# Kernel optimization log

Hardware: AMD Instinct MI355X
Metric: run time of the kernel (lower is better)

## Reference

```python
import jax, jax.numpy as jnp
import numpy as np

HEADS = 16
DIM_HEAD = 64
SCALE = DIM_HEAD ** -0.5
LN_EPS = 1e-5


def setup_inputs() -> dict:
    key = jax.random.key(0)
    k1, k2, k3 = jax.random.split(key, 3)
    b, s, d = 2, 2048, 1024
    inner = HEADS * DIM_HEAD
    x = jax.random.normal(k1, (b, s, d), dtype=jnp.float32)
    w_qkv = jax.random.normal(k2, (d, 3 * inner), dtype=jnp.float32) * (d ** -0.5)
    w_out = jax.random.normal(k3, (inner, d), dtype=jnp.float32) * (inner ** -0.5)
    return {
        "x": x,
        "ln_gamma": jnp.ones((d,), jnp.float32),
        "ln_beta": jnp.zeros((d,), jnp.float32),
        "w_qkv": w_qkv,
        "w_out": w_out,
        "b_out": jnp.zeros((d,), jnp.float32),
    }


def _layernorm(x, gamma, beta):
    mu = jnp.mean(x, axis=-1, keepdims=True)
    var = jnp.var(x, axis=-1, keepdims=True)
    return (x - mu) * jax.lax.rsqrt(var + LN_EPS) * gamma + beta


def reference(x, ln_gamma, ln_beta, w_qkv, w_out, b_out):
    b, s, d = x.shape
    xn = _layernorm(x, ln_gamma, ln_beta)
    qkv = xn @ w_qkv                       # [b, s, 3*inner]
    q, k, v = jnp.split(qkv, 3, axis=-1)
    def heads(t):
        return t.reshape(b, s, HEADS, DIM_HEAD).transpose(0, 2, 1, 3)  # [b, h, s, dh]
    q, k, v = heads(q), heads(k), heads(v)
    dots = jnp.einsum("bhqd,bhkd->bhqk", q, k) * SCALE   # [b, h, s, s]
    attn = jax.nn.softmax(dots, axis=-1)
    out = jnp.einsum("bhqk,bhkd->bhqd", attn, v)          # [b, h, s, dh]
    out = out.transpose(0, 2, 1, 3).reshape(b, s, HEADS * DIM_HEAD)
    return out @ w_out + b_out
```

## Files before the change

kernel.cpp:

```cpp
#include <hip/hip_runtime.h>
#include <hip/hip_bf16.h>
#include <stdint.h>

#define NH     16
#define DHEAD  64
#define SEQ    2048
#define DMODEL 1024
#define NBATCH 2
#define INNER  1024
#define QKVN   3072
#define ROWS   4096
#define ATT_QB 64
#define ATT_KB 64

typedef __attribute__((ext_vector_type(8))) __bf16 bf16x8;
typedef __attribute__((ext_vector_type(4))) float floatx4;
typedef __attribute__((ext_vector_type(16))) float floatx16;

__device__ __forceinline__ unsigned short f2bf(float f) {
    union { __bf16 b; unsigned short u; } c; c.b = (__bf16)f; return c.u;
}

__device__ __forceinline__ unsigned int pk2(float lo, float hi) {
    union { ushort2 s; unsigned int u; } c;
    c.s.x = f2bf(lo); c.s.y = f2bf(hi); return c.u;
}

__device__ __forceinline__ float fexp2(float x) {
#if __has_builtin(__builtin_amdgcn_exp2f)
    return __builtin_amdgcn_exp2f(x);
#else
    float r; asm("v_exp_f32 %0, %1" : "=v"(r) : "v"(x)); return r;
#endif
}

typedef __attribute__((address_space(1))) void gvoid;
typedef __attribute__((address_space(3))) void lvoid;
__device__ __forceinline__ void gl_lds16(const void* g, void* l) {
    __builtin_amdgcn_global_load_lds((gvoid*)g, (lvoid*)l, 16, 0, 0);
}

__global__ __launch_bounds__(256) void transpose_f2b(
        const float* __restrict__ in, unsigned short* __restrict__ out,
        int rows, int cols) {
    __shared__ unsigned short tile[32][33];
    const int bx = blockIdx.x * 32, by = blockIdx.y * 32;
    const int tx = threadIdx.x & 31, ty = threadIdx.x >> 5;
    for (int i = ty; i < 32; i += 8)
        tile[i][tx] = f2bf(in[(size_t)(by + i) * cols + bx + tx]);
    __syncthreads();
    for (int i = ty; i < 32; i += 8)
        out[(size_t)(bx + i) * rows + by + tx] = tile[tx][i];
}

__global__ __launch_bounds__(256) void ln_kernel(
        const float* __restrict__ x,
        const float* __restrict__ gamma,
        const float* __restrict__ beta,
        unsigned short* __restrict__ xn) {
    __shared__ float red[4][2];
    const int row = blockIdx.x, t = threadIdx.x;
    const size_t base = (size_t)row * DMODEL + t * 4;
    float4 v = *(const float4*)(x + base);
    float s  = v.x + v.y + v.z + v.w;
    float ss = v.x*v.x + v.y*v.y + v.z*v.z + v.w*v.w;
    for (int off = 32; off >= 1; off >>= 1) {
        s  += __shfl_xor(s,  off);
        ss += __shfl_xor(ss, off);
    }
    const int w = t >> 6, lane = t & 63;
    if (lane == 0) { red[w][0] = s; red[w][1] = ss; }
    __syncthreads();
    if (t == 0) {
        float S  = red[0][0] + red[1][0] + red[2][0] + red[3][0];
        float SS = red[0][1] + red[1][1] + red[2][1] + red[3][1];
        float mu  = S * (1.f / DMODEL);
        float var = SS * (1.f / DMODEL) - mu * mu;
        red[0][0] = mu; red[0][1] = rsqrtf(var + 1e-5f);
    }
    __syncthreads();
    const float mu = red[0][0], rstd = red[0][1];
    float4 g = *(const float4*)(gamma + t * 4);
    float4 bb = *(const float4*)(beta + t * 4);
    ushort4 o;
    o.x = f2bf((v.x - mu) * rstd * g.x + bb.x);
    o.y = f2bf((v.y - mu) * rstd * g.y + bb.y);
    o.z = f2bf((v.z - mu) * rstd * g.z + bb.z);
    o.w = f2bf((v.w - mu) * rstd * g.w + bb.w);
    *(ushort4*)(xn + base) = o;
}

__global__ __launch_bounds__(256) void gemm_qkv(
        const unsigned short* __restrict__ A,
        const unsigned short* __restrict__ Bt,
        unsigned short* __restrict__ qP,
        unsigned short* __restrict__ kP,
        unsigned short* __restrict__ vT) {
    const int K = DMODEL;
    __shared__ __align__(16) unsigned short sA[128 * 32];
    __shared__ __align__(16) unsigned short sB[128 * 32];
    __shared__ __align__(16) unsigned short tb[2][64 * 72];
    const int t = threadIdx.x;
    const int mBase = blockIdx.y * 128, nBase = blockIdx.x * 128;
    const int w = t >> 6, lane = t & 63, quad = lane >> 4, l16 = lane & 15;
    const int wm = (w >> 1) * 64, wn = (w & 1) * 64;
    const int srow = t >> 2, sch = t & 3;
    floatx4 acc[4][4];
    for (int mi = 0; mi < 4; mi++)
        for (int ni = 0; ni < 4; ni++) acc[mi][ni] = (floatx4)0.f;

    for (int k0 = 0; k0 < K; k0 += 32) {
        #pragma unroll
        for (int c = 0; c < 2; c++) {
            const int row = c * 64 + srow;
            const int gcol = (sch ^ ((row >> 1) & 3)) * 8;
            gl_lds16(&A[(size_t)(mBase + row) * K + k0 + gcol], &sA[(c * 256 + w * 64) * 8]);
            gl_lds16(&Bt[(size_t)(nBase + row) * K + k0 + gcol], &sB[(c * 256 + w * 64) * 8]);
        }
        __syncthreads();
        bf16x8 af[4], bfv[4];
        #pragma unroll
        for (int mi = 0; mi < 4; mi++) {
            const int r = wm + mi * 16 + l16;
            af[mi] = *(const bf16x8*)&sA[r * 32 + (quad ^ ((r >> 1) & 3)) * 8];
        }
        #pragma unroll
        for (int ni = 0; ni < 4; ni++) {
            const int r = wn + ni * 16 + l16;
            bfv[ni] = *(const bf16x8*)&sB[r * 32 + (quad ^ ((r >> 1) & 3)) * 8];
        }
        #pragma unroll
        for (int mi = 0; mi < 4; mi++)
            #pragma unroll
            for (int ni = 0; ni < 4; ni++)
                acc[mi][ni] = __builtin_amdgcn_mfma_f32_16x16x32_bf16(
                    af[mi], bfv[ni], acc[mi][ni], 0, 0, 0);
        __syncthreads();
    }
    const int reg = nBase >> 10;
    if (reg == 2) {
        #pragma unroll
        for (int ni = 0; ni < 4; ni++) {
            const int col = nBase + wn + ni * 16 + l16;
            const int h = (col & 1023) >> 6, dh = col & 63;
            #pragma unroll
            for (int mi = 0; mi < 4; mi++) {
                const int row0 = mBase + wm + mi * 16 + quad * 4;
                const int b = row0 >> 11, s0 = row0 & 2047;
                ushort4 o;
                o.x = f2bf(acc[mi][ni][0]); o.y = f2bf(acc[mi][ni][1]);
                o.z = f2bf(acc[mi][ni][2]); o.w = f2bf(acc[mi][ni][3]);
                *(ushort4*)&vT[((size_t)(b * NH + h) * DHEAD + dh) * SEQ + s0] = o;
            }
        }
    } else {
        unsigned short* dst = (reg == 0) ? qP : kP;
        const float scl = (reg == 0) ? 0.18033688011112042f : 1.f;
        const int hh = ((nBase + wn) & 1023) >> 6;
        #pragma unroll
        for (int ph = 0; ph < 2; ph++) {
            if ((w >> 1) == ph) {
                unsigned short* tb_ = &tb[w & 1][0];
                #pragma unroll
                for (int mi = 0; mi < 4; mi++)
                    #pragma unroll
                    for (int ni = 0; ni < 4; ni++)
                        #pragma unroll
                        for (int i = 0; i < 4; i++)
                            tb_[(mi * 16 + quad * 4 + i) * 72 + ni * 16 + l16] =
                                f2bf(acc[mi][ni][i] * scl);
                asm volatile("s_waitcnt lgkmcnt(0)" ::: "memory");
                const int row_g = mBase + wm + lane;
                const int b = row_g >> 11, sr = row_g & 2047;
                unsigned short* orow = dst + ((size_t)(b * NH + hh) * SEQ + sr) * DHEAD;
                #pragma unroll
                for (int c = 0; c < 8; c++)
                    *(bf16x8*)&orow[c * 8] = *(const bf16x8*)&tb_[lane * 72 + c * 8];
            }
            __syncthreads();
        }
    }
}

__global__ __launch_bounds__(256) void gemm_out(
        const unsigned short* __restrict__ A,
        const unsigned short* __restrict__ Bt,
        float* __restrict__ C,
        const int M, const int N, const int K,
        const float* __restrict__ bias) {
    __shared__ __align__(16) unsigned short sA[128 * 32];
    __shared__ __align__(16) unsigned short sB[64 * 32];
    const int t = threadIdx.x;
    const int mBase = blockIdx.y * 128, nBase = blockIdx.x * 64;
    const int w = t >> 6, lane = t & 63, quad = lane >> 4, l16 = lane & 15;
    const int wm = (w >> 1) * 64, wn = (w & 1) * 32;
    const int srow = t >> 2, sch = t & 3;
    floatx4 acc[4][2];
    for (int mi = 0; mi < 4; mi++)
        for (int ni = 0; ni < 2; ni++) acc[mi][ni] = (floatx4)0.f;

    for (int k0 = 0; k0 < K; k0 += 32) {
        #pragma unroll
        for (int c = 0; c < 2; c++) {
            const int row = c * 64 + srow;
            const int gcol = (sch ^ ((row >> 1) & 3)) * 8;
            gl_lds16(&A[(size_t)(mBase + row) * K + k0 + gcol], &sA[(c * 256 + w * 64) * 8]);
        }
        {
            const int gcol = (sch ^ ((srow >> 1) & 3)) * 8;
            gl_lds16(&Bt[(size_t)(nBase + srow) * K + k0 + gcol], &sB[(w * 64) * 8]);
        }
        __syncthreads();
        bf16x8 af[4], bfv[2];
        #pragma unroll
        for (int mi = 0; mi < 4; mi++) {
            const int r = wm + mi * 16 + l16;
            af[mi] = *(const bf16x8*)&sA[r * 32 + (quad ^ ((r >> 1) & 3)) * 8];
        }
        #pragma unroll
        for (int ni = 0; ni < 2; ni++) {
            const int r = wn + ni * 16 + l16;
            bfv[ni] = *(const bf16x8*)&sB[r * 32 + (quad ^ ((r >> 1) & 3)) * 8];
        }
        #pragma unroll
        for (int mi = 0; mi < 4; mi++)
            #pragma unroll
            for (int ni = 0; ni < 2; ni++)
                acc[mi][ni] = __builtin_amdgcn_mfma_f32_16x16x32_bf16(
                    af[mi], bfv[ni], acc[mi][ni], 0, 0, 0);
        __syncthreads();
    }
    #pragma unroll
    for (int mi = 0; mi < 4; mi++)
        #pragma unroll
        for (int ni = 0; ni < 2; ni++) {
            const int col = nBase + wn + ni * 16 + l16;
            const float badd = bias ? bias[col] : 0.f;
            #pragma unroll
            for (int i = 0; i < 4; i++) {
                const int row = mBase + wm + mi * 16 + quad * 4 + i;
                C[(size_t)row * N + col] = acc[mi][ni][i] + badd;
            }
        }
}

__global__ __launch_bounds__(256, 4) void attn_kernel(
        const unsigned short* __restrict__ qP,
        const unsigned short* __restrict__ kP,
        const unsigned short* __restrict__ vT,
        unsigned short* __restrict__ aout) {
    __shared__ __align__(16) unsigned short sK[2][ATT_KB * 64];
    __shared__ __align__(16) unsigned short sV[2][ATT_KB * 64];
    const int t = threadIdx.x, w = t >> 6, lane = t & 63;
    const int l32 = lane & 31, half = lane >> 5;
    const int qh = w & 1, kh = w >> 1;
    const int bid = blockIdx.x;
    const int xcd = bid & 7, slot = bid >> 3;
    const int bh = xcd * 4 + (slot >> 5);
    const int qb = slot & 31;
    const int b = bh >> 4, h = bh & 15;
    const int qbase = qb * ATT_QB + qh * 32;

    bf16x8 qf[4];
    #pragma unroll
    for (int kd = 0; kd < 4; kd++)
        qf[kd] = *(const bf16x8*)&qP[
            ((size_t)bh * SEQ + qbase + l32) * DHEAD + kd * 16 + half * 8];

    floatx16 oac[2];
    oac[0] = (floatx16)0.f; oac[1] = (floatx16)0.f;
    float lS = 0.f;

    const unsigned short* kb = kP + (size_t)bh * SEQ * DHEAD;
    const unsigned short* vb = vT + (size_t)bh * DHEAD * SEQ;
    const int r8 = lane >> 3, sw8 = ((lane & 7) ^ r8) * 8;

    auto stage = [&](int it, int bi) {
        const int kv0 = it * ATT_KB;
        #pragma unroll
        for (int ii = 0; ii < 2; ii++) {
            const int row = w * 16 + ii * 8 + r8;
            gl_lds16(kb + (size_t)(kv0 + row) * DHEAD + sw8,
                     (void*)&sK[bi][(w * 16 + ii * 8) * 64]);
            gl_lds16(vb + (size_t)row * SEQ + kv0 + sw8,
                     (void*)&sV[bi][(w * 16 + ii * 8) * 64]);
        }
    };
    stage(0, 0);

    const int NIT = SEQ / ATT_KB;
    for (int it = 0; it < NIT; ++it) {
        __syncthreads();
        const int bi = it & 1;
        if (it + 1 < NIT) stage(it + 1, bi ^ 1);

        bf16x8 kf[4];
        #pragma unroll
        for (int kd = 0; kd < 4; kd++) {
            const int r = kh * 32 + l32;
            kf[kd] = *(const bf16x8*)&sK[bi][r * 64 + 8 * ((2 * kd + half) ^ (l32 & 7))];
        }

        floatx16 sv = (floatx16)0.f;
        __builtin_amdgcn_s_setprio(1);
        #pragma unroll
        for (int kd = 0; kd < 4; kd++)
            sv = __builtin_amdgcn_mfma_f32_32x32x16_bf16(kf[kd], qf[kd], sv, 0, 0, 0);
        __builtin_amdgcn_s_setprio(0);

        float p[16];
        #pragma unroll
        for (int i = 0; i < 16; i++) p[i] = fexp2(sv[i]);
        {
            float s = 0.f;
            #pragma unroll
            for (int i = 0; i < 16; i++) s += p[i];
            s += __shfl_xor(s, 32);
            lS += s;
        }

        bf16x8 pf[2];
        #pragma unroll
        for (int kd = 0; kd < 2; kd++) {
            const int base = kd * 8;
            unsigned int c01 = pk2(p[base + 0], p[base + 1]);
            unsigned int c23 = pk2(p[base + 2], p[base + 3]);
            unsigned int c45 = pk2(p[base + 4], p[base + 5]);
            unsigned int c67 = pk2(p[base + 6], p[base + 7]);
            asm("v_permlane32_swap_b32 %0, %1" : "+v"(c01), "+v"(c45));
            asm("v_permlane32_swap_b32 %0, %1" : "+v"(c23), "+v"(c67));
            union { unsigned int u[4]; bf16x8 v; } fr;
            fr.u[0] = c01; fr.u[1] = c23; fr.u[2] = c45; fr.u[3] = c67;
            pf[kd] = fr.v;
        }

        __builtin_amdgcn_s_setprio(1);
        #pragma unroll
        for (int dt = 0; dt < 2; dt++)
            #pragma unroll
            for (int kd = 0; kd < 2; kd++) {
                const int r = dt * 32 + l32;
                bf16x8 vf = *(const bf16x8*)&sV[bi][
                    r * 64 + 8 * ((kh * 4 + kd * 2 + half) ^ (l32 & 7))];
                oac[dt] = __builtin_amdgcn_mfma_f32_32x32x16_bf16(vf, pf[kd], oac[dt], 0, 0, 0);
            }
        __builtin_amdgcn_s_setprio(0);
    }

    __syncthreads();
    float* redO = (float*)&sK[0][0];
    float* redL = (float*)&sV[0][0];
    if (kh == 1) {
        #pragma unroll
        for (int dt = 0; dt < 2; dt++)
            #pragma unroll
            for (int g = 0; g < 4; g++) {
                const int c = dt * 4 + g;
                float4 o4;
                o4.x = oac[dt][g * 4 + 0]; o4.y = oac[dt][g * 4 + 1];
                o4.z = oac[dt][g * 4 + 2]; o4.w = oac[dt][g * 4 + 3];
                *(float4*)&redO[((size_t)qh * 64 + lane) * 32 + 4 * (c ^ (lane & 7))] = o4;
            }
        if (half == 0) redL[qh * 32 + l32] = lS;
    }
    __syncthreads();
    if (kh == 0) {
        #pragma unroll
        for (int dt = 0; dt < 2; dt++)
            #pragma unroll
            for (int g = 0; g < 4; g++) {
                const int c = dt * 4 + g;
                float4 o4 = *(const float4*)&redO[
                    ((size_t)qh * 64 + lane) * 32 + 4 * (c ^ (lane & 7))];
                oac[dt][g * 4 + 0] += o4.x; oac[dt][g * 4 + 1] += o4.y;
                oac[dt][g * 4 + 2] += o4.z; oac[dt][g * 4 + 3] += o4.w;
            }
        lS += redL[qh * 32 + l32];
        const float rl = 1.f / lS;
        unsigned short* orow = aout + ((size_t)(b * SEQ + qbase + l32)) * INNER + h * DHEAD;
        #pragma unroll
        for (int dt = 0; dt < 2; dt++)
            #pragma unroll
            for (int g = 0; g < 4; g++) {
                ushort4 o;
                o.x = f2bf(oac[dt][g * 4 + 0] * rl);
                o.y = f2bf(oac[dt][g * 4 + 1] * rl);
                o.z = f2bf(oac[dt][g * 4 + 2] * rl);
                o.w = f2bf(oac[dt][g * 4 + 3] * rl);
                *(ushort4*)&orow[dt * 32 + g * 8 + half * 4] = o;
            }
    }
}

extern "C" void kernel_launch(void* const* d_in, const int* in_sizes, int n_in,
                              void* d_out, int out_size, void* d_ws, size_t ws_size,
                              hipStream_t stream) {
    const float* x     = (const float*)d_in[0];
    const float* gamma = (const float*)d_in[1];
    const float* beta  = (const float*)d_in[2];
    const float* wqkv  = (const float*)d_in[3];
    const float* wout  = (const float*)d_in[4];
    const float* bout  = (const float*)d_in[5];
    float* out = (float*)d_out;

    unsigned short* ws     = (unsigned short*)d_ws;
    unsigned short* xn     = ws;
    unsigned short* wqkvT  = xn     + (size_t)ROWS * DMODEL;
    unsigned short* qPb    = wqkvT  + (size_t)QKVN * DMODEL;
    unsigned short* kPb    = qPb    + (size_t)NBATCH * NH * SEQ * DHEAD;
    unsigned short* vTb    = kPb    + (size_t)NBATCH * NH * SEQ * DHEAD;
    unsigned short* attnO  = vTb    + (size_t)NBATCH * NH * SEQ * DHEAD;
    unsigned short* woutT  = attnO  + (size_t)ROWS * INNER;

    transpose_f2b<<<dim3(QKVN / 32, DMODEL / 32), 256, 0, stream>>>(wqkv, wqkvT, DMODEL, QKVN);
    transpose_f2b<<<dim3(DMODEL / 32, INNER / 32), 256, 0, stream>>>(wout, woutT, INNER, DMODEL);
    ln_kernel<<<ROWS, 256, 0, stream>>>(x, gamma, beta, xn);
    gemm_qkv<<<dim3(QKVN / 128, ROWS / 128), 256, 0, stream>>>(xn, wqkvT, qPb, kPb, vTb);
    attn_kernel<<<dim3((SEQ / ATT_QB) * NBATCH * NH), 256, 0, stream>>>(
        qPb, kPb, vTb, attnO);
    gemm_out<<<dim3(DMODEL / 64, ROWS / 128), 256, 0, stream>>>(
        attnO, woutT, out, ROWS, DMODEL, INNER, bout);
}
```

Before: 213.1 us.

## Double GEMM K-tile to 64 with 8-way XOR swizzle and merge weight transposes

Both GEMMs now stage 64-wide K slices in LDS per iteration instead of 32, with an 8-chunk XOR swizzle, so each sync pair covers twice as many MFMAs and the number of K-loop iterations and barriers is halved. The two weight transpose launches are merged into one kernel using a z-dimension grid, saving a launch. LDS usage doubles for the GEMMs, which may lower occupancy. The merged transpose launches many early-exit blocks for the smaller matrix.

Result: faster. 201.9 us (-5.2%).

```diff
diff --git a/kernel.cpp b/kernel.cpp
--- a/kernel.cpp
+++ b/kernel.cpp
@@ -40,10 +40,16 @@
     __builtin_amdgcn_global_load_lds((gvoid*)g, (lvoid*)l, 16, 0, 0);
 }
 
-__global__ __launch_bounds__(256) void transpose_f2b(
-        const float* __restrict__ in, unsigned short* __restrict__ out,
-        int rows, int cols) {
+__global__ __launch_bounds__(256) void transpose_two(
+        const float* __restrict__ inA, unsigned short* __restrict__ outA,
+        const float* __restrict__ inB, unsigned short* __restrict__ outB) {
     __shared__ unsigned short tile[32][33];
+    const float* in; unsigned short* out; int rows, cols;
+    if (blockIdx.z == 0) { in = inA; out = outA; rows = DMODEL; cols = QKVN; }
+    else {
+        if (blockIdx.x >= DMODEL / 32) return;
+        in = inB; out = outB; rows = INNER; cols = DMODEL;
+    }
     const int bx = blockIdx.x * 32, by = blockIdx.y * 32;
     const int tx = threadIdx.x & 31, ty = threadIdx.x >> 5;
     for (int i = ty; i < 32; i += 8)
@@ -97,44 +103,47 @@
         unsigned short* __restrict__ kP,
         unsigned short* __restrict__ vT) {
     const int K = DMODEL;
-    __shared__ __align__(16) unsigned short sA[128 * 32];
-    __shared__ __align__(16) unsigned short sB[128 * 32];
+    __shared__ __align__(16) unsigned short sA[128 * 64];
+    __shared__ __align__(16) unsigned short sB[128 * 64];
     __shared__ __align__(16) unsigned short tb[2][64 * 72];
     const int t = threadIdx.x;
     const int mBase = blockIdx.y * 128, nBase = blockIdx.x * 128;
     const int w = t >> 6, lane = t & 63, quad = lane >> 4, l16 = lane & 15;
     const int wm = (w >> 1) * 64, wn = (w & 1) * 64;
-    const int srow = t >> 2, sch = t & 3;
+    const int srow8 = lane >> 3;
+    const int gcol = ((lane & 7) ^ srow8) * 8;
     floatx4 acc[4][4];
     for (int mi = 0; mi < 4; mi++)
         for (int ni = 0; ni < 4; ni++) acc[mi][ni] = (floatx4)0.f;
 
-    for (int k0 = 0; k0 < K; k0 += 32) {
-        #pragma unroll
-        for (int c = 0; c < 2; c++) {
-            const int row = c * 64 + srow;
-            const int gcol = (sch ^ ((row >> 1) & 3)) * 8;
-            gl_lds16(&A[(size_t)(mBase + row) * K + k0 + gcol], &sA[(c * 256 + w * 64) * 8]);
-            gl_lds16(&Bt[(size_t)(nBase + row) * K + k0 + gcol], &sB[(c * 256 + w * 64) * 8]);
+    for (int k0 = 0; k0 < K; k0 += 64) {
+        #pragma unroll
+        for (int c = 0; c < 4; c++) {
+            const int row = c * 32 + w * 8 + srow8;
+            gl_lds16(&A[(size_t)(mBase + row) * K + k0 + gcol], &sA[(c * 32 + w * 8) * 64]);
+            gl_lds16(&Bt[(size_t)(nBase + row) * K + k0 + gcol], &sB[(c * 32 + w * 8) * 64]);
         }
         __syncthreads();
-        bf16x8 af[4], bfv[4];
-        #pragma unroll
-        for (int mi = 0; mi < 4; mi++) {
-            const int r = wm + mi * 16 + l16;
-            af[mi] = *(const bf16x8*)&sA[r * 32 + (quad ^ ((r >> 1) & 3)) * 8];
-        }
-        #pragma unroll
-        for (int ni = 0; ni < 4; ni++) {
-            const int r = wn + ni * 16 + l16;
-            bfv[ni] = *(const bf16x8*)&sB[r * 32 + (quad ^ ((r >> 1) & 3)) * 8];
-        }
-        #pragma unroll
-        for (int mi = 0; mi < 4; mi++)
-            #pragma unroll
-            for (int ni = 0; ni < 4; ni++)
-                acc[mi][ni] = __builtin_amdgcn_mfma_f32_16x16x32_bf16(
-                    af[mi], bfv[ni], acc[mi][ni], 0, 0, 0);
+        #pragma unroll
+        for (int s = 0; s < 2; s++) {
+            bf16x8 af[4], bfv[4];
+            #pragma unroll
+            for (int mi = 0; mi < 4; mi++) {
+                const int r = wm + mi * 16 + l16;
+                af[mi] = *(const bf16x8*)&sA[r * 64 + (((s << 2) | quad) ^ (r & 7)) * 8];
+            }
+            #pragma unroll
+            for (int ni = 0; ni < 4; ni++) {
+                const int r = wn + ni * 16 + l16;
+                bfv[ni] = *(const bf16x8*)&sB[r * 64 + (((s << 2) | quad) ^ (r & 7)) * 8];
+            }
+            #pragma unroll
+            for (int mi = 0; mi < 4; mi++)
+                #pragma unroll
+                for (int ni = 0; ni < 4; ni++)
+                    acc[mi][ni] = __builtin_amdgcn_mfma_f32_16x16x32_bf16(
+                        af[mi], bfv[ni], acc[mi][ni], 0, 0, 0);
+        }
         __syncthreads();
     }
     const int reg = nBase >> 10;
@@ -188,46 +197,50 @@
         float* __restrict__ C,
         const int M, const int N, const int K,
         const float* __restrict__ bias) {
-    __shared__ __align__(16) unsigned short sA[128 * 32];
-    __shared__ __align__(16) unsigned short sB[64 * 32];
+    __shared__ __align__(16) unsigned short sA[128 * 64];
+    __shared__ __align__(16) unsigned short sB[64 * 64];
     const int t = threadIdx.x;
     const int mBase = blockIdx.y * 128, nBase = blockIdx.x * 64;
     const int w = t >> 6, lane = t & 63, quad = lane >> 4, l16 = lane & 15;
     const int wm = (w >> 1) * 64, wn = (w & 1) * 32;
-    const int srow = t >> 2, sch = t & 3;
+    const int srow8 = lane >> 3;
+    const int gcol = ((lane & 7) ^ srow8) * 8;
     floatx4 acc[4][2];
     for (int mi = 0; mi < 4; mi++)
         for (int ni = 0; ni < 2; ni++) acc[mi][ni] = (floatx4)0.f;
 
-    for (int k0 = 0; k0 < K; k0 += 32) {
+    for (int k0 = 0; k0 < K; k0 += 64) {
+        #pragma unroll
+        for (int c = 0; c < 4; c++) {
+            const int row = c * 32 + w * 8 + srow8;
+            gl_lds16(&A[(size_t)(mBase + row) * K + k0 + gcol], &sA[(c * 32 + w * 8) * 64]);
+        }
         #pragma unroll
         for (int c = 0; c < 2; c++) {
-            const int row = c * 64 + srow;
-            const int gcol = (sch ^ ((row >> 1) & 3)) * 8;
-            gl_lds16(&A[(size_t)(mBase + row) * K + k0 + gcol], &sA[(c * 256 + w * 64) * 8]);
-        }
-        {
-            const int gcol = (sch ^ ((srow >> 1) & 3)) * 8;
-            gl_lds16(&Bt[(size_t)(nBase + srow) * K + k0 + gcol], &sB[(w * 64) * 8]);
+            const int row = c * 32 + w * 8 + srow8;
+            gl_lds16(&Bt[(size_t)(nBase + row) * K + k0 + gcol], &sB[(c * 32 + w * 8) * 64]);
         }
         __syncthreads();
-        bf16x8 af[4], bfv[2];
-        #pragma unroll
-        for (int mi = 0; mi < 4; mi++) {
-            const int r = wm + mi * 16 + l16;
-            af[mi] = *(const bf16x8*)&sA[r * 32 + (quad ^ ((r >> 1) & 3)) * 8];
-        }
-        #pragma unroll
-        for (int ni = 0; ni < 2; ni++) {
-            const int r = wn + ni * 16 + l16;
-            bfv[ni] = *(const bf16x8*)&sB[r * 32 + (quad ^ ((r >> 1) & 3)) * 8];
-        }
-        #pragma unroll
-        for (int mi = 0; mi < 4; mi++)
-            #pragma unroll
-            for (int ni = 0; ni < 2; ni++)
-                acc[mi][ni] = __builtin_amdgcn_mfma_f32_16x16x32_bf16(
-                    af[mi], bfv[ni], acc[mi][ni], 0, 0, 0);
+        #pragma unroll
+        for (int s = 0; s < 2; s++) {
+            bf16x8 af[4], bfv[2];
+            #pragma unroll
+            for (int mi = 0; mi < 4; mi++) {
+                const int r = wm + mi * 16 + l16;
+                af[mi] = *(const bf16x8*)&sA[r * 64 + (((s << 2) | quad) ^ (r & 7)) * 8];
+            }
+            #pragma unroll
+            for (int ni = 0; ni < 2; ni++) {
+                const int r = wn + ni * 16 + l16;
+                bfv[ni] = *(const bf16x8*)&sB[r * 64 + (((s << 2) | quad) ^ (r & 7)) * 8];
+            }
+            #pragma unroll
+            for (int mi = 0; mi < 4; mi++)
+                #pragma unroll
+                for (int ni = 0; ni < 2; ni++)
+                    acc[mi][ni] = __builtin_amdgcn_mfma_f32_16x16x32_bf16(
+                        af[mi], bfv[ni], acc[mi][ni], 0, 0, 0);
+        }
         __syncthreads();
     }
     #pragma unroll
@@ -412,8 +425,8 @@
     unsigned short* attnO  = vTb    + (size_t)NBATCH * NH * SEQ * DHEAD;
     unsigned short* woutT  = attnO  + (size_t)ROWS * INNER;
 
-    transpose_f2b<<<dim3(QKVN / 32, DMODEL / 32), 256, 0, stream>>>(wqkv, wqkvT, DMODEL, QKVN);
-    transpose_f2b<<<dim3(DMODEL / 32, INNER / 32), 256, 0, stream>>>(wout, woutT, INNER, DMODEL);
+    transpose_two<<<dim3(QKVN / 32, DMODEL / 32, 2), 256, 0, stream>>>(
+        wqkv, wqkvT, wout, woutT);
     ln_kernel<<<ROWS, 256, 0, stream>>>(x, gamma, beta, xn);
     gemm_qkv<<<dim3(QKVN / 128, ROWS / 128), 256, 0, stream>>>(xn, wqkvT, qPb, kPb, vTb);
     attn_kernel<<<dim3((SEQ / ATT_QB) * NBATCH * NH), 256, 0, stream>>>(
```

## Double-buffer LDS tiles in both GEMMs and merge weight transposes into one launch

Applied to the files above, without the earlier changes.

Both GEMM kernels now use two LDS buffers, issuing the global-to-LDS loads for the next K step before computing on the current one, so load latency overlaps with MFMA work. gemm_qkv reuses the staging buffer for its epilogue transpose, which saves LDS. The two weight transpose launches are merged into one kernel using blockIdx.z, removing a launch. Doubling LDS may lower occupancy, and the ordering of async loads against the remaining barrier needs care.

New measurement: 210.8 us. Within noise of the previous version (-1.1%).

```diff
diff --git a/kernel.cpp b/kernel.cpp
--- a/kernel.cpp
+++ b/kernel.cpp
@@ -40,10 +40,16 @@
     __builtin_amdgcn_global_load_lds((gvoid*)g, (lvoid*)l, 16, 0, 0);
 }
 
-__global__ __launch_bounds__(256) void transpose_f2b(
-        const float* __restrict__ in, unsigned short* __restrict__ out,
-        int rows, int cols) {
+__global__ __launch_bounds__(256) void transpose_two(
+        const float* __restrict__ inA, unsigned short* __restrict__ outA,
+        const float* __restrict__ inB, unsigned short* __restrict__ outB) {
     __shared__ unsigned short tile[32][33];
+    const float* in; unsigned short* out; int rows, cols;
+    if (blockIdx.z == 0) { in = inA; out = outA; rows = DMODEL; cols = QKVN; }
+    else {
+        if (blockIdx.x >= DMODEL / 32) return;
+        in = inB; out = outB; rows = INNER; cols = DMODEL;
+    }
     const int bx = blockIdx.x * 32, by = blockIdx.y * 32;
     const int tx = threadIdx.x & 31, ty = threadIdx.x >> 5;
     for (int i = ty; i < 32; i += 8)
@@ -97,9 +103,7 @@
         unsigned short* __restrict__ kP,
         unsigned short* __restrict__ vT) {
     const int K = DMODEL;
-    __shared__ __align__(16) unsigned short sA[128 * 32];
-    __shared__ __align__(16) unsigned short sB[128 * 32];
-    __shared__ __align__(16) unsigned short tb[2][64 * 72];
+    __shared__ __align__(16) unsigned short sbuf[2][2][128 * 32];
     const int t = threadIdx.x;
     const int mBase = blockIdx.y * 128, nBase = blockIdx.x * 128;
     const int w = t >> 6, lane = t & 63, quad = lane >> 4, l16 = lane & 15;
@@ -109,15 +113,26 @@
     for (int mi = 0; mi < 4; mi++)
         for (int ni = 0; ni < 4; ni++) acc[mi][ni] = (floatx4)0.f;
 
-    for (int k0 = 0; k0 < K; k0 += 32) {
+    auto stage = [&](int k0, int bi) {
         #pragma unroll
         for (int c = 0; c < 2; c++) {
             const int row = c * 64 + srow;
             const int gcol = (sch ^ ((row >> 1) & 3)) * 8;
-            gl_lds16(&A[(size_t)(mBase + row) * K + k0 + gcol], &sA[(c * 256 + w * 64) * 8]);
-            gl_lds16(&Bt[(size_t)(nBase + row) * K + k0 + gcol], &sB[(c * 256 + w * 64) * 8]);
-        }
-        __syncthreads();
+            gl_lds16(&A[(size_t)(mBase + row) * K + k0 + gcol],
+                     &sbuf[bi][0][(c * 256 + w * 64) * 8]);
+            gl_lds16(&Bt[(size_t)(nBase + row) * K + k0 + gcol],
+                     &sbuf[bi][1][(c * 256 + w * 64) * 8]);
+        }
+    };
+    stage(0, 0);
+    __syncthreads();
+
+    const int NK = K / 32;
+    for (int kk = 0; kk < NK; ++kk) {
+        const int bi = kk & 1;
+        if (kk + 1 < NK) stage((kk + 1) * 32, bi ^ 1);
+        const unsigned short* sA = &sbuf[bi][0][0];
+        const unsigned short* sB = &sbuf[bi][1][0];
         bf16x8 af[4], bfv[4];
         #pragma unroll
         for (int mi = 0; mi < 4; mi++) {
@@ -157,10 +172,11 @@
         unsigned short* dst = (reg == 0) ? qP : kP;
         const float scl = (reg == 0) ? 0.18033688011112042f : 1.f;
         const int hh = ((nBase + wn) & 1023) >> 6;
+        unsigned short* tb0 = &sbuf[0][0][0];
         #pragma unroll
         for (int ph = 0; ph < 2; ph++) {
             if ((w >> 1) == ph) {
-                unsigned short* tb_ = &tb[w & 1][0];
+                unsigned short* tb_ = tb0 + (w & 1) * (64 * 72);
                 #pragma unroll
                 for (int mi = 0; mi < 4; mi++)
                     #pragma unroll
@@ -188,8 +204,8 @@
         float* __restrict__ C,
         const int M, const int N, const int K,
         const float* __restrict__ bias) {
-    __shared__ __align__(16) unsigned short sA[128 * 32];
-    __shared__ __align__(16) unsigned short sB[64 * 32];
+    __shared__ __align__(16) unsigned short sAb[2][128 * 32];
+    __shared__ __align__(16) unsigned short sBb[2][64 * 32];
     const int t = threadIdx.x;
     const int mBase = blockIdx.y * 128, nBase = blockIdx.x * 64;
     const int w = t >> 6, lane = t & 63, quad = lane >> 4, l16 = lane & 15;
@@ -199,18 +215,29 @@
     for (int mi = 0; mi < 4; mi++)
         for (int ni = 0; ni < 2; ni++) acc[mi][ni] = (floatx4)0.f;
 
-    for (int k0 = 0; k0 < K; k0 += 32) {
+    auto stage = [&](int k0, int bi) {
         #pragma unroll
         for (int c = 0; c < 2; c++) {
             const int row = c * 64 + srow;
             const int gcol = (sch ^ ((row >> 1) & 3)) * 8;
-            gl_lds16(&A[(size_t)(mBase + row) * K + k0 + gcol], &sA[(c * 256 + w * 64) * 8]);
+            gl_lds16(&A[(size_t)(mBase + row) * K + k0 + gcol],
+                     &sAb[bi][(c * 256 + w * 64) * 8]);
         }
         {
             const int gcol = (sch ^ ((srow >> 1) & 3)) * 8;
-            gl_lds16(&Bt[(size_t)(nBase + srow) * K + k0 + gcol], &sB[(w * 64) * 8]);
-        }
-        __syncthreads();
+            gl_lds16(&Bt[(size_t)(nBase + srow) * K + k0 + gcol],
+                     &sBb[bi][(w * 64) * 8]);
+        }
+    };
+    stage(0, 0);
+    __syncthreads();
+
+    const int NK = K / 32;
+    for (int kk = 0; kk < NK; ++kk) {
+        const int bi = kk & 1;
+        if (kk + 1 < NK) stage((kk + 1) * 32, bi ^ 1);
+        const unsigned short* sA = &sAb[bi][0];
+        const unsigned short* sB = &sBb[bi][0];
         bf16x8 af[4], bfv[2];
         #pragma unroll
         for (int mi = 0; mi < 4; mi++) {
@@ -412,8 +439,8 @@
     unsigned short* attnO  = vTb    + (size_t)NBATCH * NH * SEQ * DHEAD;
     unsigned short* woutT  = attnO  + (size_t)ROWS * INNER;
 
-    transpose_f2b<<<dim3(QKVN / 32, DMODEL / 32), 256, 0, stream>>>(wqkv, wqkvT, DMODEL, QKVN);
-    transpose_f2b<<<dim3(DMODEL / 32, INNER / 32), 256, 0, stream>>>(wout, woutT, INNER, DMODEL);
+    transpose_two<<<dim3(QKVN / 32, DMODEL / 32, 2), 256, 0, stream>>>(
+        wqkv, wqkvT, wout, woutT);
     ln_kernel<<<ROWS, 256, 0, stream>>>(x, gamma, beta, xn);
     gemm_qkv<<<dim3(QKVN / 128, ROWS / 128), 256, 0, stream>>>(xn, wqkvT, qPb, kPb, vTb);
     attn_kernel<<<dim3((SEQ / ATT_QB) * NBATCH * NH), 256, 0, stream>>>(
```

## Merge prep kernels and triple-buffer LDS staging in both GEMMs

Applied to the files above, without the earlier changes.

Folds the two weight transposes and the layernorm into one launch, using a 3D grid where the z index picks the job. Both GEMMs now keep three LDS buffers and prefetch two k-steps ahead with global_load_lds, waiting on partial vmcnt so there is one barrier per step instead of two. The QKV epilogue reuses the staging LDS so all four waves transpose at once rather than in two phases. The cost is more LDS per block, which may reduce occupancy, and correctness depends on the hand-counted vmcnt values.

After: 195.0 us. 8.5% less time.

```diff
diff --git a/kernel.cpp b/kernel.cpp
--- a/kernel.cpp
+++ b/kernel.cpp
@@ -40,54 +40,63 @@
     __builtin_amdgcn_global_load_lds((gvoid*)g, (lvoid*)l, 16, 0, 0);
 }
 
-__global__ __launch_bounds__(256) void transpose_f2b(
-        const float* __restrict__ in, unsigned short* __restrict__ out,
-        int rows, int cols) {
+__global__ __launch_bounds__(256) void prep_kernel(
+        const float* __restrict__ x,
+        const float* __restrict__ gamma,
+        const float* __restrict__ beta,
+        unsigned short* __restrict__ xn,
+        const float* __restrict__ wqkv, unsigned short* __restrict__ wqkvT,
+        const float* __restrict__ wout, unsigned short* __restrict__ woutT) {
     __shared__ unsigned short tile[32][33];
+    __shared__ float red[4][2];
+    const int t = threadIdx.x;
+    if (blockIdx.z == 2) {
+        const int row = blockIdx.y * 128 + blockIdx.x;
+        const size_t base = (size_t)row * DMODEL + t * 4;
+        float4 v = *(const float4*)(x + base);
+        float s  = v.x + v.y + v.z + v.w;
+        float ss = v.x*v.x + v.y*v.y + v.z*v.z + v.w*v.w;
+        for (int off = 32; off >= 1; off >>= 1) {
+            s  += __shfl_xor(s,  off);
+            ss += __shfl_xor(ss, off);
+        }
+        const int w = t >> 6, lane = t & 63;
+        if (lane == 0) { red[w][0] = s; red[w][1] = ss; }
+        __syncthreads();
+        if (t == 0) {
+            float S  = red[0][0] + red[1][0] + red[2][0] + red[3][0];
+            float SS = red[0][1] + red[1][1] + red[2][1] + red[3][1];
+            float mu  = S * (1.f / DMODEL);
+            float var = SS * (1.f / DMODEL) - mu * mu;
+            red[0][0] = mu; red[0][1] = rsqrtf(var + 1e-5f);
+        }
+        __syncthreads();
+        const float mu = red[0][0], rstd = red[0][1];
+        float4 g = *(const float4*)(gamma + t * 4);
+        float4 bb = *(const float4*)(beta + t * 4);
+        ushort4 o;
+        o.x = f2bf((v.x - mu) * rstd * g.x + bb.x);
+        o.y = f2bf((v.y - mu) * rstd * g.y + bb.y);
+        o.z = f2bf((v.z - mu) * rstd * g.z + bb.z);
+        o.w = f2bf((v.w - mu) * rstd * g.w + bb.w);
+        *(ushort4*)(xn + base) = o;
+        return;
+    }
+    const float* in; unsigned short* out; int rows, cols;
+    if (blockIdx.z == 0) {
+        if (blockIdx.x >= QKVN / 32) return;
+        in = wqkv; out = wqkvT; rows = DMODEL; cols = QKVN;
+    } else {
+        if (blockIdx.x >= DMODEL / 32) return;
+        in = wout; out = woutT; rows = INNER; cols = DMODEL;
+    }
     const int bx = blockIdx.x * 32, by = blockIdx.y * 32;
-    const int tx = threadIdx.x & 31, ty = threadIdx.x >> 5;
+    const int tx = t & 31, ty = t >> 5;
     for (int i = ty; i < 32; i += 8)
         tile[i][tx] = f2bf(in[(size_t)(by + i) * cols + bx + tx]);
     __syncthreads();
     for (int i = ty; i < 32; i += 8)
         out[(size_t)(bx + i) * rows + by + tx] = tile[tx][i];
-}
-
-__global__ __launch_bounds__(256) void ln_kernel(
-        const float* __restrict__ x,
-        const float* __restrict__ gamma,
-        const float* __restrict__ beta,
-        unsigned short* __restrict__ xn) {
-    __shared__ float red[4][2];
-    const int row = blockIdx.x, t = threadIdx.x;
-    const size_t base = (size_t)row * DMODEL + t * 4;
-    float4 v = *(const float4*)(x + base);
-    float s  = v.x + v.y + v.z + v.w;
-    float ss = v.x*v.x + v.y*v.y + v.z*v.z + v.w*v.w;
-    for (int off = 32; off >= 1; off >>= 1) {
-        s  += __shfl_xor(s,  off);
-        ss += __shfl_xor(ss, off);
-    }
-    const int w = t >> 6, lane = t & 63;
-    if (lane == 0) { red[w][0] = s; red[w][1] = ss; }
-    __syncthreads();
-    if (t == 0) {
-        float S  = red[0][0] + red[1][0] + red[2][0] + red[3][0];
-        float SS = red[0][1] + red[1][1] + red[2][1] + red[3][1];
-        float mu  = S * (1.f / DMODEL);
-        float var = SS * (1.f / DMODEL) - mu * mu;
-        red[0][0] = mu; red[0][1] = rsqrtf(var + 1e-5f);
-    }
-    __syncthreads();
-    const float mu = red[0][0], rstd = red[0][1];
-    float4 g = *(const float4*)(gamma + t * 4);
-    float4 bb = *(const float4*)(beta + t * 4);
-    ushort4 o;
-    o.x = f2bf((v.x - mu) * rstd * g.x + bb.x);
-    o.y = f2bf((v.y - mu) * rstd * g.y + bb.y);
-    o.z = f2bf((v.z - mu) * rstd * g.z + bb.z);
-    o.w = f2bf((v.w - mu) * rstd * g.w + bb.w);
-    *(ushort4*)(xn + base) = o;
 }
 
 __global__ __launch_bounds__(256) void gemm_qkv(
@@ -97,9 +106,7 @@
         unsigned short* __restrict__ kP,
         unsigned short* __restrict__ vT) {
     const int K = DMODEL;
-    __shared__ __align__(16) unsigned short sA[128 * 32];
-    __shared__ __align__(16) unsigned short sB[128 * 32];
-    __shared__ __align__(16) unsigned short tb[2][64 * 72];
+    __shared__ __align__(16) unsigned short smem[3 * 8192];
     const int t = threadIdx.x;
     const int mBase = blockIdx.y * 128, nBase = blockIdx.x * 128;
     const int w = t >> 6, lane = t & 63, quad = lane >> 4, l16 = lane & 15;
@@ -109,7 +116,9 @@
     for (int mi = 0; mi < 4; mi++)
         for (int ni = 0; ni < 4; ni++) acc[mi][ni] = (floatx4)0.f;
 
-    for (int k0 = 0; k0 < K; k0 += 32) {
+    auto stage = [&](int k0, int bi) {
+        unsigned short* sA = smem + bi * 8192;
+        unsigned short* sB = sA + 4096;
         #pragma unroll
         for (int c = 0; c < 2; c++) {
             const int row = c * 64 + srow;
@@ -117,7 +126,19 @@
             gl_lds16(&A[(size_t)(mBase + row) * K + k0 + gcol], &sA[(c * 256 + w * 64) * 8]);
             gl_lds16(&Bt[(size_t)(nBase + row) * K + k0 + gcol], &sB[(c * 256 + w * 64) * 8]);
         }
-        __syncthreads();
+    };
+
+    const int NK = K / 32;
+    stage(0, 0);
+    stage(32, 1);
+    for (int kk = 0; kk < NK; ++kk) {
+        if (kk + 1 < NK) { asm volatile("s_waitcnt vmcnt(4)" ::: "memory"); }
+        else             { asm volatile("s_waitcnt vmcnt(0)" ::: "memory"); }
+        __builtin_amdgcn_sched_barrier(0);
+        __builtin_amdgcn_s_barrier();
+        if (kk + 2 < NK) stage((kk + 2) * 32, (kk + 2) % 3);
+        const unsigned short* sA = smem + (kk % 3) * 8192;
+        const unsigned short* sB = sA + 4096;
         bf16x8 af[4], bfv[4];
         #pragma unroll
         for (int mi = 0; mi < 4; mi++) {
@@ -135,8 +156,8 @@
             for (int ni = 0; ni < 4; ni++)
                 acc[mi][ni] = __builtin_amdgcn_mfma_f32_16x16x32_bf16(
                     af[mi], bfv[ni], acc[mi][ni], 0, 0, 0);
-        __syncthreads();
-    }
+    }
+    __syncthreads();
     const int reg = nBase >> 10;
     if (reg == 2) {
         #pragma unroll
@@ -157,28 +178,22 @@
         unsigned short* dst = (reg == 0) ? qP : kP;
         const float scl = (reg == 0) ? 0.18033688011112042f : 1.f;
         const int hh = ((nBase + wn) & 1023) >> 6;
-        #pragma unroll
-        for (int ph = 0; ph < 2; ph++) {
-            if ((w >> 1) == ph) {
-                unsigned short* tb_ = &tb[w & 1][0];
+        unsigned short* tb_ = smem + w * (64 * 72);
+        #pragma unroll
+        for (int mi = 0; mi < 4; mi++)
+            #pragma unroll
+            for (int ni = 0; ni < 4; ni++)
                 #pragma unroll
-                for (int mi = 0; mi < 4; mi++)
-                    #pragma unroll
-                    for (int ni = 0; ni < 4; ni++)
-                        #pragma unroll
-                        for (int i = 0; i < 4; i++)
-                            tb_[(mi * 16 + quad * 4 + i) * 72 + ni * 16 + l16] =
-                                f2bf(acc[mi][ni][i] * scl);
-                asm volatile("s_waitcnt lgkmcnt(0)" ::: "memory");
-                const int row_g = mBase + wm + lane;
-                const int b = row_g >> 11, sr = row_g & 2047;
-                unsigned short* orow = dst + ((size_t)(b * NH + hh) * SEQ + sr) * DHEAD;
-                #pragma unroll
-                for (int c = 0; c < 8; c++)
-                    *(bf16x8*)&orow[c * 8] = *(const bf16x8*)&tb_[lane * 72 + c * 8];
-            }
-            __syncthreads();
-        }
+                for (int i = 0; i < 4; i++)
+                    tb_[(mi * 16 + quad * 4 + i) * 72 + ni * 16 + l16] =
+                        f2bf(acc[mi][ni][i] * scl);
+        asm volatile("s_waitcnt lgkmcnt(0)" ::: "memory");
+        const int row_g = mBase + wm + lane;
+        const int b = row_g >> 11, sr = row_g & 2047;
+        unsigned short* orow = dst + ((size_t)(b * NH + hh) * SEQ + sr) * DHEAD;
+        #pragma unroll
+        for (int c = 0; c < 8; c++)
+            *(bf16x8*)&orow[c * 8] = *(const bf16x8*)&tb_[lane * 72 + c * 8];
     }
 }
 
@@ -188,8 +203,7 @@
         float* __restrict__ C,
         const int M, const int N, const int K,
         const float* __restrict__ bias) {
-    __shared__ __align__(16) unsigned short sA[128 * 32];
-    __shared__ __align__(16) unsigned short sB[64 * 32];
+    __shared__ __align__(16) unsigned short smem[3 * 6144];
     const int t = threadIdx.x;
     const int mBase = blockIdx.y * 128, nBase = blockIdx.x * 64;
     const int w = t >> 6, lane = t & 63, quad = lane >> 4, l16 = lane & 15;
@@ -199,7 +213,9 @@
     for (int mi = 0; mi < 4; mi++)
         for (int ni = 0; ni < 2; ni++) acc[mi][ni] = (floatx4)0.f;
 
-    for (int k0 = 0; k0 < K; k0 += 32) {
+    auto stage = [&](int k0, int bi) {
+        unsigned short* sA = smem + bi * 6144;
+        unsigned short* sB = sA + 4096;
         #pragma unroll
         for (int c = 0; c < 2; c++) {
             const int row = c * 64 + srow;
@@ -210,7 +226,19 @@
             const int gcol = (sch ^ ((srow >> 1) & 3)) * 8;
             gl_lds16(&Bt[(size_t)(nBase + srow) * K + k0 + gcol], &sB[(w * 64) * 8]);
         }
-        __syncthreads();
+    };
+
+    const int NK = K / 32;
+    stage(0, 0);
+    stage(32, 1);
+    for (int kk = 0; kk < NK; ++kk) {
+        if (kk + 1 < NK) { asm volatile("s_waitcnt vmcnt(3)" ::: "memory"); }
+        else             { asm volatile("s_waitcnt vmcnt(0)" ::: "memory"); }
+        __builtin_amdgcn_sched_barrier(0);
+        __builtin_amdgcn_s_barrier();
+        if (kk + 2 < NK) stage((kk + 2) * 32, (kk + 2) % 3);
+        const unsigned short* sA = smem + (kk % 3) * 6144;
+        const unsigned short* sB = sA + 4096;
         bf16x8 af[4], bfv[2];
         #pragma unroll
         for (int mi = 0; mi < 4; mi++) {
@@ -228,7 +256,6 @@
             for (int ni = 0; ni < 2; ni++)
                 acc[mi][ni] = __builtin_amdgcn_mfma_f32_16x16x32_bf16(
                     af[mi], bfv[ni], acc[mi][ni], 0, 0, 0);
-        __syncthreads();
     }
     #pragma unroll
     for (int mi = 0; mi < 4; mi++)
@@ -412,9 +439,8 @@
     unsigned short* attnO  = vTb    + (size_t)NBATCH * NH * SEQ * DHEAD;
     unsigned short* woutT  = attnO  + (size_t)ROWS * INNER;
 
-    transpose_f2b<<<dim3(QKVN / 32, DMODEL / 32), 256, 0, stream>>>(wqkv, wqkvT, DMODEL, QKVN);
-    transpose_f2b<<<dim3(DMODEL / 32, INNER / 32), 256, 0, stream>>>(wout, woutT, INNER, DMODEL);
-    ln_kernel<<<ROWS, 256, 0, stream>>>(x, gamma, beta, xn);
+    prep_kernel<<<dim3(128, 32, 3), 256, 0, stream>>>(
+        x, gamma, beta, xn, wqkv, wqkvT, wout, woutT);
     gemm_qkv<<<dim3(QKVN / 128, ROWS / 128), 256, 0, stream>>>(xn, wqkvT, qPb, kPb, vTb);
     attn_kernel<<<dim3((SEQ / ATT_QB) * NBATCH * NH), 256, 0, stream>>>(
         qPb, kPb, vTb, attnO);
```
